# Kernel tuning notes

Measured on AMD Instinct MI355X. Metric: run time of the kernel, lower is better.

## Reference

```python
import jax, jax.numpy as jnp
import numpy as np

NUM_LEVELS = 4
RADIUS = 4


def setup_inputs() -> dict:
    key = jax.random.key(0)
    k1, k2, k3 = jax.random.split(key, 3)
    B, C, H, W = 2, 256, 64, 64
    N = 4
    fmap1 = jax.random.normal(k1, (B, C, H, W), dtype=jnp.float32)
    fmap2 = jax.random.normal(k2, (B, C, H, W), dtype=jnp.float32)
    # coords channel 0 = x in [0, W-1], channel 1 = y in [0, H-1]
    coords = jax.random.uniform(k3, (B, N, 2, H, W), dtype=jnp.float32) * (W - 1)
    return {"fmap1": fmap1, "fmap2": fmap2, "coords": coords}


def _bilinear_gather(corr, x, y):
    """Zero-padded bilinear sampling (grid_sample align_corners=True semantics).
    corr: (B, P, h2, w2) per-query-pixel correlation maps.
    x, y: (B, N, P, K2) absolute pixel coords into (w2, h2).
    Returns (B, N, P, K2)."""
    Bv, P, h2, w2 = corr.shape
    x0 = jnp.floor(x)
    y0 = jnp.floor(y)
    wx1 = x - x0
    wy1 = y - y0
    b = jnp.arange(Bv)[:, None, None, None]
    p = jnp.arange(P)[None, None, :, None]

    def corner(yi, xi):
        valid = (xi >= 0) & (xi <= w2 - 1) & (yi >= 0) & (yi <= h2 - 1)
        xi_c = jnp.clip(xi, 0, w2 - 1).astype(jnp.int32)
        yi_c = jnp.clip(yi, 0, h2 - 1).astype(jnp.int32)
        v = corr[b, p, yi_c, xi_c]
        return jnp.where(valid, v, jnp.zeros((), corr.dtype))

    v00 = corner(y0, x0)
    v01 = corner(y0, x0 + 1)
    v10 = corner(y0 + 1, x0)
    v11 = corner(y0 + 1, x0 + 1)
    return ((1 - wy1) * (1 - wx1) * v00 + (1 - wy1) * wx1 * v01
            + wy1 * (1 - wx1) * v10 + wy1 * wx1 * v11)


def reference(fmap1, fmap2, coords):
    B, C, H, W = fmap1.shape
    _, N = coords.shape[0], coords.shape[1]
    P = H * W
    r = RADIUS
    K = 2 * r + 1
    K2 = K * K

    # All-pairs correlation: (B, P_query, H2, W2), scaled by 1/sqrt(C) (RAFT)
    f1 = fmap1.reshape(B, C, P)
    f2 = fmap2.reshape(B, C, P)
    corr = jnp.einsum('bcp,bcq->bpq', f1, f2) / jnp.sqrt(jnp.asarray(C, fmap1.dtype))
    corr = corr.reshape(B, P, H, W)

    # Pyramid via 2x2 average pooling (stride 2, no padding)
    pyramid = [corr]
    c = corr
    for _ in range(NUM_LEVELS - 1):
        h2, w2 = c.shape[-2:]
        c = c.reshape(B, P, h2 // 2, 2, w2 // 2, 2).mean(axis=(3, 5))
        pyramid.append(c)

    # Window offsets. Faithful to the torch code: delta = stack(meshgrid(dy, dx, 'ij'))
    # so delta[...,0] = yy is added to the x-channel, delta[...,1] = xx to the y-channel.
    d = jnp.linspace(-r, r, K).astype(coords.dtype)
    yy, xx = jnp.meshgrid(d, d, indexing='ij')
    off_x = yy.reshape(1, 1, 1, K2)  # added to coords[...,0]
    off_y = xx.reshape(1, 1, 1, K2)  # added to coords[...,1]

    cx = coords[:, :, 0].reshape(B, N, P)  # (B, N, P)
    cy = coords[:, :, 1].reshape(B, N, P)

    outs = []
    for i, cl in enumerate(pyramid):
        scale = jnp.asarray(2.0 ** i, coords.dtype)
        x = cx[..., None] / scale + off_x  # (B, N, P, K2)
        y = cy[..., None] / scale + off_y
        v = _bilinear_gather(cl, x, y)     # (B, N, P, K2)
        outs.append(v.reshape(B, N, H, W, K2))

    out = jnp.concatenate(outs, axis=-1)   # (B, N, H, W, L*K2)
    Ctot = out.shape[-1]
    # Matches torch: contiguous (B,N,H,W,C) reshaped row-major to (B, N*C, H, W)
    out = out.reshape(B, N * Ctot, H, W)
    return out.astype(jnp.float32)
```

## Files before the change

kernel.cpp:

```cpp
#include <hip/hip_runtime.h>
#include <hip/hip_bf16.h>
#include <cstdint>

#define B_    2
#define C_    256
#define H_    64
#define W_    64
#define P_    (H_*W_)
#define N_    4
#define RAD   4
#define K2_   81
#define CTOT  (4*K2_)

typedef __bf16 bf16x8 __attribute__((ext_vector_type(8)));
typedef float  f32x4  __attribute__((ext_vector_type(4)));

__device__ __forceinline__ void gload_lds16(const void* g, void* l) {
    __builtin_amdgcn_global_load_lds(
        (const __attribute__((address_space(1))) void*)g,
        (__attribute__((address_space(3))) void*)l,
        16, 0, 0);
}

__global__ void transpose_cvt(const float* __restrict__ in0,
                              const float* __restrict__ in1,
                              __hip_bfloat16* __restrict__ out0,
                              __hip_bfloat16* __restrict__ out1) {
    __shared__ float tile[32][33];
    const int z     = blockIdx.z;
    const int which = z >> 1;
    const int b     = z & 1;
    const float* in          = which ? in1  : in0;
    __hip_bfloat16* out      = which ? out1 : out0;
    const int p0 = blockIdx.x * 32;
    const int c0 = blockIdx.y * 32;
    const int tx = threadIdx.x;
    const int ty = threadIdx.y;
    const float* src = in + ((size_t)b * C_ + c0) * P_ + p0;
    #pragma unroll
    for (int i = 0; i < 32; i += 8)
        tile[ty + i][tx] = src[(size_t)(ty + i) * P_ + tx];
    __syncthreads();
    __hip_bfloat16* dst = out + ((size_t)b * P_ + p0) * C_ + c0;
    #pragma unroll
    for (int i = 0; i < 32; i += 8)
        dst[(size_t)(ty + i) * C_ + tx] = __float2bfloat16(tile[tx][ty + i]);
}

#define TSTR 136

__global__ __launch_bounds__(256) void gemm_corr(
    const short* __restrict__ f1t,
    const short* __restrict__ f2t,
    __hip_bfloat16* __restrict__ corr0,
    __hip_bfloat16* __restrict__ corr1)
{
    __shared__ short smem[128 * TSTR];
    short* As = smem;
    short* Bs = smem + 8192;

    const int tid  = threadIdx.x;
    const int lane = tid & 63;
    const int wv   = tid >> 6;
    const int wm   = (wv >> 1) * 64;
    const int wn   = (wv & 1) * 64;
    const int b    = blockIdx.z;
    const int bx   = blockIdx.x;
    const int m0   = blockIdx.y * 128;
    const int n0   = bx * 128;
    const int qd   = lane >> 4;
    const int l15  = lane & 15;

    const short* gA[4];
    const short* gB[4];
    int ldsOff[4];
    #pragma unroll
    for (int it = 0; it < 4; ++it) {
        const int ci = it * 256 + tid;
        const int r  = ci >> 3;
        const int cp = ci & 7;
        const int kc = cp ^ (r & 7);
        gA[it] = f1t + ((size_t)(b * P_ + m0 + r)) * C_ + kc * 8;
        gB[it] = f2t + ((size_t)(b * P_ + n0 + r)) * C_ + kc * 8;
        ldsOff[it] = (it * 256 + wv * 64) * 8;
    }

    int aAddr[4][2], bAddr[4][2];
    #pragma unroll
    for (int i = 0; i < 4; ++i) {
        const int m = wm + i * 16 + l15;
        const int n = wn + i * 16 + l15;
        #pragma unroll
        for (int s = 0; s < 2; ++s) {
            const int lc = s * 4 + qd;
            aAddr[i][s] = m * 64 + ((lc ^ (m & 7)) * 8);
            bAddr[i][s] = n * 64 + ((lc ^ (n & 7)) * 8);
        }
    }

    f32x4 zero = {0.f, 0.f, 0.f, 0.f};
    f32x4 acc[4][4];
    #pragma unroll
    for (int mi = 0; mi < 4; ++mi)
        #pragma unroll
        for (int ni = 0; ni < 4; ++ni)
            acc[mi][ni] = zero;

    for (int kt = 0; kt < 4; ++kt) {
        const int k0 = kt * 64;
        #pragma unroll
        for (int it = 0; it < 4; ++it) {
            gload_lds16(gA[it] + k0, As + ldsOff[it]);
            gload_lds16(gB[it] + k0, Bs + ldsOff[it]);
        }
        __syncthreads();
        #pragma unroll
        for (int s = 0; s < 2; ++s) {
            bf16x8 af[4], bfr[4];
            #pragma unroll
            for (int i = 0; i < 4; ++i) {
                af[i]  = *(const bf16x8*)(As + aAddr[i][s]);
                bfr[i] = *(const bf16x8*)(Bs + bAddr[i][s]);
            }
            #pragma unroll
            for (int mi = 0; mi < 4; ++mi)
                #pragma unroll
                for (int ni = 0; ni < 4; ++ni)
                    acc[mi][ni] = __builtin_amdgcn_mfma_f32_16x16x32_bf16(
                        af[mi], bfr[ni], acc[mi][ni], 0, 0, 0);
        }
        __syncthreads();
    }

    const float sc = 0.0625f;
    __hip_bfloat16* tile = (__hip_bfloat16*)smem;
    #pragma unroll
    for (int mi = 0; mi < 4; ++mi) {
        #pragma unroll
        for (int ni = 0; ni < 4; ++ni) {
            #pragma unroll
            for (int r = 0; r < 4; ++r) {
                const int rl = wm + mi * 16 + qd * 4 + r;
                const int cl = wn + ni * 16 + l15;
                tile[rl * TSTR + cl] = __float2bfloat16(acc[mi][ni][r] * sc);
            }
        }
    }
    __syncthreads();

    #pragma unroll
    for (int i = 0; i < 8; ++i) {
        const int cid = i * 256 + tid;
        const int tr  = cid >> 4;
        const int tc  = cid & 15;
        const float4 v = *(const float4*)(smem + tr * TSTR + tc * 8);
        *(float4*)(corr0 + ((size_t)(b * P_ + m0 + tr)) * P_ + n0 + tc * 8) = v;
    }

    #pragma unroll
    for (int i = 0; i < 16; ++i) {
        const int oid = i * 256 + tid;
        const int pr  = oid >> 5;
        const int pc  = oid & 31;
        const uint32_t u0 = *(const uint32_t*)(smem + pr * TSTR + 2 * pc);
        const uint32_t u1 = *(const uint32_t*)(smem + pr * TSTR + 64 + 2 * pc);
        const float a0 = __uint_as_float(u0 << 16);
        const float a1 = __uint_as_float(u0 & 0xffff0000u);
        const float b0 = __uint_as_float(u1 << 16);
        const float b1 = __uint_as_float(u1 & 0xffff0000u);
        corr1[((size_t)(b * P_ + m0 + pr)) * 1024 + bx * 32 + pc] =
            __float2bfloat16((a0 + a1 + b0 + b1) * 0.25f);
    }
}

__global__ __launch_bounds__(256) void gather5(
    const float* __restrict__ coords,
    const __hip_bfloat16* __restrict__ c0,
    const __hip_bfloat16* __restrict__ c1,
    float* __restrict__ out) {
    __shared__ float pool_sm[320];
    __shared__ float patch[4][440];

    const int tid  = threadIdx.x;
    const int lane = tid & 63;
    const int n    = tid >> 6;
    const int bp   = blockIdx.x;
    const int b    = bp >> 12;
    const int p    = bp & (P_ - 1);

    const __hip_bfloat16* c0b = c0 + (size_t)bp * 4096;
    const __hip_bfloat16* c1b = c1 + (size_t)bp * 1024;

    const float cx = coords[((size_t)((b * N_ + n) * 2 + 0)) * P_ + p];
    const float cy = coords[((size_t)((b * N_ + n) * 2 + 1)) * P_ + p];
    int x0i[4], y0i[4];
    float w00[4], w01[4], w10[4], w11[4];
    #pragma unroll
    for (int l = 0; l < 4; ++l) {
        const float inv = (l == 0) ? 1.f : (l == 1) ? 0.5f : (l == 2) ? 0.25f : 0.125f;
        const float x = cx * inv, y = cy * inv;
        const float x0f = floorf(x), y0f = floorf(y);
        const float wx = x - x0f, wy = y - y0f;
        x0i[l] = (int)x0f - RAD;
        y0i[l] = (int)y0f - RAD;
        w00[l] = (1.f - wy) * (1.f - wx);
        w01[l] = (1.f - wy) * wx;
        w10[l] = wy * (1.f - wx);
        w11[l] = wy * wx;
    }

    float pv[2][2];
    #pragma unroll
    for (int lvl = 0; lvl < 2; ++lvl) {
        const __hip_bfloat16* src = lvl ? c1b : c0b;
        const int hw = lvl ? 32 : 64;
        const int sh = lvl ? 5 : 6;
        #pragma unroll
        for (int it = 0; it < 2; ++it) {
            const int idx = it * 64 + lane;
            const int r   = idx / 11;
            const int cc  = idx - r * 11;
            const int gr  = y0i[lvl] + r, gc = x0i[lvl] + cc;
            float v = 0.f;
            if ((idx < 110) & (cc < 10) & ((unsigned)gr < (unsigned)hw) &
                ((unsigned)gc < (unsigned)hw))
                v = __bfloat162float(src[(gr << sh) + gc]);
            pv[lvl][it] = v;
        }
    }

    {
        const int y2 = tid >> 4, x2 = tid & 15;
        const uint32_t u0 = *(const uint32_t*)(c1b + (2 * y2) * 32 + 2 * x2);
        const uint32_t u1 = *(const uint32_t*)(c1b + (2 * y2 + 1) * 32 + 2 * x2);
        const float a0 = __uint_as_float(u0 << 16);
        const float a1 = __uint_as_float(u0 & 0xffff0000u);
        const float b0 = __uint_as_float(u1 << 16);
        const float b1 = __uint_as_float(u1 & 0xffff0000u);
        pool_sm[tid] = (a0 + a1 + b0 + b1) * 0.25f;
    }
    __syncthreads();
    if (tid < 64) {
        const int y3 = tid >> 3, x3 = tid & 7;
        const float* r0 = pool_sm + (2 * y3) * 16 + 2 * x3;
        pool_sm[256 + tid] = (r0[0] + r0[1] + r0[16] + r0[17]) * 0.25f;
    }
    __syncthreads();

    float* pw = patch[n];
    #pragma unroll
    for (int lvl = 0; lvl < 2; ++lvl) {
        #pragma unroll
        for (int it = 0; it < 2; ++it) {
            const int idx = it * 64 + lane;
            if (idx < 110) pw[lvl * 110 + idx] = pv[lvl][it];
        }
    }
    #pragma unroll
    for (int lvl = 2; lvl < 4; ++lvl) {
        const int hw   = (lvl == 2) ? 16 : 8;
        const int sh   = (lvl == 2) ? 4 : 3;
        const int base = (lvl == 2) ? 0 : 256;
        #pragma unroll
        for (int it = 0; it < 2; ++it) {
            const int idx = it * 64 + lane;
            if (idx < 110) {
                const int r  = idx / 11;
                const int cc = idx - r * 11;
                const int gr = y0i[lvl] + r, gc = x0i[lvl] + cc;
                float v = 0.f;
                if ((cc < 10) & ((unsigned)gr < (unsigned)hw) &
                    ((unsigned)gc < (unsigned)hw))
                    v = pool_sm[base + (gr << sh) + gc];
                pw[lvl * 110 + idx] = v;
            }
        }
    }

    const size_t obase = ((size_t)(b * N_ + n) * P_ + p) * CTOT;
    #pragma unroll
    for (int lvl = 0; lvl < 4; ++lvl) {
        const float* pl = pw + lvl * 110;
        float* ol = out + obase + lvl * K2_;
        #pragma unroll
        for (int it = 0; it < 2; ++it) {
            const int k2 = it * 64 + lane;
            if (k2 < K2_) {
                const int ki = k2 / 9;
                const int kj = k2 - ki * 9;
                const float* pr = pl + kj * 11 + ki;
                ol[k2] = w00[lvl] * pr[0] + w01[lvl] * pr[1] +
                         w10[lvl] * pr[11] + w11[lvl] * pr[12];
            }
        }
    }
}

extern "C" void kernel_launch(void* const* d_in, const int* in_sizes, int n_in,
                              void* d_out, int out_size, void* d_ws, size_t ws_size,
                              hipStream_t stream) {
    const float* fmap1  = (const float*)d_in[0];
    const float* fmap2  = (const float*)d_in[1];
    const float* coords = (const float*)d_in[2];
    float* out = (float*)d_out;

    char* ws = (char*)d_ws;
    __hip_bfloat16* f1t = (__hip_bfloat16*)ws;
    __hip_bfloat16* f2t = (__hip_bfloat16*)(ws + 4194304);
    __hip_bfloat16* c0  = (__hip_bfloat16*)(ws + 8388608);
    __hip_bfloat16* c1  = (__hip_bfloat16*)(ws + 75497472);

    {
        dim3 grid(P_ / 32, C_ / 32, 2 * B_);
        dim3 blk(32, 8);
        transpose_cvt<<<grid, blk, 0, stream>>>(fmap1, fmap2, f1t, f2t);
    }

    {
        dim3 grid(P_ / 128, P_ / 128, B_);
        gemm_corr<<<grid, 256, 0, stream>>>((const short*)f1t, (const short*)f2t,
                                            c0, c1);
    }

    gather5<<<B_ * P_, 256, 0, stream>>>(coords, c0, c1, out);
}
```

Measured before the change: 124.8 us.

## Extract level-0 sampling windows in GEMM epilogue instead of storing full corr

```diff
diff --git a/kernel.cpp b/kernel.cpp
--- a/kernel.cpp
+++ b/kernel.cpp
@@ -52,8 +52,9 @@
 __global__ __launch_bounds__(256) void gemm_corr(
     const short* __restrict__ f1t,
     const short* __restrict__ f2t,
-    __hip_bfloat16* __restrict__ corr0,
-    __hip_bfloat16* __restrict__ corr1)
+    const float* __restrict__ coords,
+    __hip_bfloat16* __restrict__ corr1,
+    __hip_bfloat16* __restrict__ patch0)
 {
     __shared__ short smem[128 * TSTR];
     short* As = smem;
@@ -147,15 +148,6 @@
         }
     }
     __syncthreads();
-
-    #pragma unroll
-    for (int i = 0; i < 8; ++i) {
-        const int cid = i * 256 + tid;
-        const int tr  = cid >> 4;
-        const int tc  = cid & 15;
-        const float4 v = *(const float4*)(smem + tr * TSTR + tc * 8);
-        *(float4*)(corr0 + ((size_t)(b * P_ + m0 + tr)) * P_ + n0 + tc * 8) = v;
-    }
 
     #pragma unroll
     for (int i = 0; i < 16; ++i) {
@@ -171,11 +163,38 @@
         corr1[((size_t)(b * P_ + m0 + pr)) * 1024 + bx * 32 + pc] =
             __float2bfloat16((a0 + a1 + b0 + b1) * 0.25f);
     }
-}
-
-__global__ __launch_bounds__(256) void gather5(
+
+    const int row0 = 2 * bx;
+    #pragma unroll
+    for (int pair0 = 0; pair0 < 2; ++pair0) {
+        const int pair = pair0 * 256 + tid;
+        const int n    = pair & 3;
+        const int pi   = pair >> 2;
+        const int p    = m0 + pi;
+        const float cx = coords[((size_t)((b * N_ + n) * 2 + 0)) * P_ + p];
+        const float cy = coords[((size_t)((b * N_ + n) * 2 + 1)) * P_ + p];
+        const int x0 = (int)floorf(cx) - RAD;
+        const int y0 = (int)floorf(cy) - RAD;
+        __hip_bfloat16* pd = patch0 + ((size_t)(b * P_ + p) * N_ + n) * 110;
+        #pragma unroll
+        for (int rr = 0; rr < 2; ++rr) {
+            const int kj = (row0 + rr) - y0;
+            if ((unsigned)kj < 10u) {
+                const __hip_bfloat16* ts = tile + pi * TSTR + rr * 64;
+                #pragma unroll
+                for (int ki = 0; ki < 10; ++ki) {
+                    const int gc = x0 + ki;
+                    if ((unsigned)gc < 64u)
+                        pd[kj * 11 + ki] = ts[gc];
+                }
+            }
+        }
+    }
+}
+
+__global__ __launch_bounds__(256) void gather6(
     const float* __restrict__ coords,
-    const __hip_bfloat16* __restrict__ c0,
+    const __hip_bfloat16* __restrict__ patch0g,
     const __hip_bfloat16* __restrict__ c1,
     float* __restrict__ out) {
     __shared__ float pool_sm[320];
@@ -188,7 +207,6 @@
     const int b    = bp >> 12;
     const int p    = bp & (P_ - 1);
 
-    const __hip_bfloat16* c0b = c0 + (size_t)bp * 4096;
     const __hip_bfloat16* c1b = c1 + (size_t)bp * 1024;
 
     const float cx = coords[((size_t)((b * N_ + n) * 2 + 0)) * P_ + p];
@@ -210,23 +228,32 @@
     }
 
     float pv[2][2];
-    #pragma unroll
-    for (int lvl = 0; lvl < 2; ++lvl) {
-        const __hip_bfloat16* src = lvl ? c1b : c0b;
-        const int hw = lvl ? 32 : 64;
-        const int sh = lvl ? 5 : 6;
+    {
+        const __hip_bfloat16* p0 = patch0g + ((size_t)bp * N_ + n) * 110;
         #pragma unroll
         for (int it = 0; it < 2; ++it) {
             const int idx = it * 64 + lane;
             const int r   = idx / 11;
             const int cc  = idx - r * 11;
-            const int gr  = y0i[lvl] + r, gc = x0i[lvl] + cc;
+            const int gr  = y0i[0] + r, gc = x0i[0] + cc;
             float v = 0.f;
-            if ((idx < 110) & (cc < 10) & ((unsigned)gr < (unsigned)hw) &
-                ((unsigned)gc < (unsigned)hw))
-                v = __bfloat162float(src[(gr << sh) + gc]);
-            pv[lvl][it] = v;
-        }
+            if ((idx < 110) & (cc < 10) & ((unsigned)gr < 64u) &
+                ((unsigned)gc < 64u))
+                v = __bfloat162float(p0[idx]);
+            pv[0][it] = v;
+        }
+    }
+    #pragma unroll
+    for (int it = 0; it < 2; ++it) {
+        const int idx = it * 64 + lane;
+        const int r   = idx / 11;
+        const int cc  = idx - r * 11;
+        const int gr  = y0i[1] + r, gc = x0i[1] + cc;
+        float v = 0.f;
+        if ((idx < 110) & (cc < 10) & ((unsigned)gr < 32u) &
+            ((unsigned)gc < 32u))
+            v = __bfloat162float(c1b[(gr << 5) + gc]);
+        pv[1][it] = v;
     }
 
     {
@@ -305,10 +332,10 @@
     float* out = (float*)d_out;
 
     char* ws = (char*)d_ws;
-    __hip_bfloat16* f1t = (__hip_bfloat16*)ws;
-    __hip_bfloat16* f2t = (__hip_bfloat16*)(ws + 4194304);
-    __hip_bfloat16* c0  = (__hip_bfloat16*)(ws + 8388608);
-    __hip_bfloat16* c1  = (__hip_bfloat16*)(ws + 75497472);
+    __hip_bfloat16* f1t    = (__hip_bfloat16*)ws;
+    __hip_bfloat16* f2t    = (__hip_bfloat16*)(ws + 4194304);
+    __hip_bfloat16* c1     = (__hip_bfloat16*)(ws + 8388608);
+    __hip_bfloat16* patch0 = (__hip_bfloat16*)(ws + 25165824);
 
     {
         dim3 grid(P_ / 32, C_ / 32, 2 * B_);
@@ -319,8 +346,8 @@
     {
         dim3 grid(P_ / 128, P_ / 128, B_);
         gemm_corr<<<grid, 256, 0, stream>>>((const short*)f1t, (const short*)f2t,
-                                            c0, c1);
-    }
-
-    gather5<<<B_ * P_, 256, 0, stream>>>(coords, c0, c1, out);
-}
+                                            coords, c1, patch0);
+    }
+
+    gather6<<<B_ * P_, 256, 0, stream>>>(coords, patch0, c1, out);
+}
```

After: 133.3 us. +6.8%, slower.
